# Kernel tuning notes

Hardware: AMD Instinct MI355X
Metric: run time of the kernel (lower is better)

Reference implementation:

```python
import jax, jax.numpy as jnp
import numpy as np

N = 6000          # nodes
E = 192000        # edges (avg degree 32)
D = 512           # input_dim
H = 512           # hidden_dim
O = 40            # output_dim (classes)
K = 4096          # codebook_size
LAMB_EDGE = 1.0
LAMB_NODE = 1.0
COMMIT_W = 0.25
EPS = 1e-12


def _graph_conv(x, W, b, src, dst):
    """DGL GraphConv with norm='both' + ReLU activation.
    out = relu( D_in^{-1/2} A D_out^{-1/2} x W + b )"""
    ones = jnp.ones((E,), x.dtype)
    deg_out = jnp.clip(jax.ops.segment_sum(ones, src, num_segments=N), 1.0)
    deg_in = jnp.clip(jax.ops.segment_sum(ones, dst, num_segments=N), 1.0)
    xs = x * jax.lax.rsqrt(deg_out)[:, None]          # scale by src out-degree
    agg = jax.ops.segment_sum(xs[src], dst, num_segments=N)  # gather-scatter
    agg = agg * jax.lax.rsqrt(deg_in)[:, None]        # scale by dst in-degree
    return jax.nn.relu(agg @ W + b)


def _l2norm(x):
    return x * jax.lax.rsqrt(jnp.sum(x * x, axis=-1, keepdims=True) + EPS)


def setup_inputs() -> dict:
    key = jax.random.key(0)
    ks = jax.random.split(key, 13)
    s = lambda d: 1.0 / np.sqrt(d)
    return {
        "feats": jax.random.normal(ks[0], (N, D), jnp.float32),
        "W1": jax.random.normal(ks[1], (D, D), jnp.float32) * s(D),
        "b1": jnp.zeros((D,), jnp.float32),
        "W2": jax.random.normal(ks[2], (D, H), jnp.float32) * s(D),
        "b2": jnp.zeros((H,), jnp.float32),
        "Wd1": jax.random.normal(ks[3], (D, D), jnp.float32) * s(D),
        "bd1": jnp.zeros((D,), jnp.float32),
        "Wd2": jax.random.normal(ks[4], (D, D), jnp.float32) * s(D),
        "bd2": jnp.zeros((D,), jnp.float32),
        "Wl": jax.random.normal(ks[5], (H, O), jnp.float32) * s(H),
        "bl": jnp.zeros((O,), jnp.float32),
        "codebook": jax.random.normal(ks[6], (K, D), jnp.float32),
        "src": jax.random.randint(ks[7], (E,), 0, N, jnp.int32),
        "dst": jax.random.randint(ks[8], (E,), 0, N, jnp.int32),
    }


def reference(feats, W1, b1, W2, b2, Wd1, bd1, Wd2, bd2, Wl, bl, codebook, src, dst):
    # dense adjacency (as the torch module materializes via to_dense())
    adj = jnp.zeros((N, N), feats.dtype).at[dst, src].add(1.0)

    # GraphConv layer 1 (dropout is identity in eval)
    h = _graph_conv(feats, W1, b1, src, dst)           # [N, D]

    # cosine-sim VectorQuantize
    hn = _l2norm(h)
    en = _l2norm(codebook)                             # [K, D]
    dist = hn @ en.T                                   # [N, K] cosine sims
    ind = jnp.argmax(dist, axis=-1)                    # [N]
    q = en[ind]                                        # quantize with normed codebook
    commit_loss = COMMIT_W * jnp.mean((jax.lax.stop_gradient(q) - h) ** 2)
    quantized = h + jax.lax.stop_gradient(q - h)       # straight-through

    quantized_edge = quantized @ Wd1 + bd1             # decoder_1
    quantized_node = quantized @ Wd2 + bd2             # decoder_2

    feature_rec_loss = LAMB_NODE * jnp.mean((h - quantized_node) ** 2)

    adj_q = quantized_edge @ quantized_edge.T          # [N, N]
    adj_q = (adj_q - adj_q.min()) / (adj_q.max() - adj_q.min())
    edge_rec_loss = LAMB_EDGE * jnp.sqrt(jnp.mean((adj - adj_q) ** 2))

    # GraphConv layer 2 + output linear
    h2 = _graph_conv(quantized_edge, W2, b2, src, dst) # [N, H]
    out = h2 @ Wl + bl                                 # [N, O]

    loss = feature_rec_loss + edge_rec_loss + commit_loss
    return out, loss, dist
```

## Files before the change

### kernel.cpp

```cpp
#include <hip/hip_runtime.h>

typedef unsigned int u32;
typedef unsigned long long u64;

#define NN_ 6000
#define EE_ 192000
#define DD_ 512
#define KK_ 4096
#define OO_ 40
#define HSZ (1 << 19)
#define HMASK (HSZ - 1)
#define MT_A 376
#define NB_N 47

typedef __bf16 bf16x8 __attribute__((ext_vector_type(8)));
typedef float f32x4 __attribute__((ext_vector_type(4)));

__device__ __forceinline__ u32 okey(float f) {
    u32 u = __float_as_uint(f);
    return (u & 0x80000000u) ? ~u : (u | 0x80000000u);
}
__device__ __forceinline__ float dkey(u32 u) {
    u32 b = (u & 0x80000000u) ? (u ^ 0x80000000u) : ~u;
    return __uint_as_float(b);
}
__device__ __forceinline__ u64 packKey(float v, int col) {
    return ((u64)okey(v) << 32) | (u32)(~(u32)col);
}
__device__ __forceinline__ unsigned short f2bf_rne(float f) {
    u32 x = __float_as_uint(f);
    u32 r = x + 0x7fffu + ((x >> 16) & 1u);
    return (unsigned short)(r >> 16);
}
__device__ __forceinline__ void gld_lds16(void* l, const void* g) {
    __builtin_amdgcn_global_load_lds(
        (const __attribute__((address_space(1))) unsigned int*)g,
        (__attribute__((address_space(3))) unsigned int*)l, 16, 0, 0);
}
#define LGKM0 do { asm volatile("s_waitcnt lgkmcnt(0)" ::: "memory"); __builtin_amdgcn_sched_barrier(0); } while (0)

__global__ void k_deg(const int* __restrict__ src, const int* __restrict__ dst,
                      int* __restrict__ degout, int* __restrict__ degin) {
    int e = blockIdx.x * 256 + threadIdx.x;
    if (e >= EE_) return;
    atomicAdd(&degout[src[e]], 1);
    atomicAdd(&degin[dst[e]], 1);
}

__global__ void k_rsqrtdeg(const int* __restrict__ degout, const int* __restrict__ degin,
                           float* __restrict__ rout, float* __restrict__ rin) {
    int i = blockIdx.x * 256 + threadIdx.x;
    if (i >= NN_) return;
    int doV = degout[i]; if (doV < 1) doV = 1;
    int diV = degin[i];  if (diV < 1) diV = 1;
    rout[i] = rsqrtf((float)doV);
    rin[i]  = rsqrtf((float)diV);
}

__global__ void k_scan(const int* __restrict__ cnt, int* __restrict__ offs, int n) {
    __shared__ int buf[1024];
    __shared__ int carry;
    if (threadIdx.x == 0) { carry = 0; offs[0] = 0; }
    __syncthreads();
    for (int base = 0; base < n; base += 1024) {
        int i = base + threadIdx.x;
        int v = (i < n) ? cnt[i] : 0;
        buf[threadIdx.x] = v;
        __syncthreads();
        for (int off = 1; off < 1024; off <<= 1) {
            int t = (threadIdx.x >= off) ? buf[threadIdx.x - off] : 0;
            __syncthreads();
            buf[threadIdx.x] += t;
            __syncthreads();
        }
        if (i < n) offs[i + 1] = carry + buf[threadIdx.x];
        __syncthreads();
        if (threadIdx.x == 0) carry += buf[1023];
        __syncthreads();
    }
}

__global__ void k_fill(const int* __restrict__ src, const int* __restrict__ dst,
                       const int* __restrict__ offs, int* __restrict__ cursor,
                       int* __restrict__ esrc) {
    int e = blockIdx.x * 256 + threadIdx.x;
    if (e >= EE_) return;
    int d = dst[e];
    int pos = offs[d] + atomicAdd(&cursor[d], 1);
    esrc[pos] = src[e];
}

__device__ __forceinline__ void split8(const float* vals, uint4& hw, uint4& lw) {
    u32 h[4], l[4];
    #pragma unroll
    for (int j = 0; j < 4; ++j) {
        unsigned short h0 = f2bf_rne(vals[2*j]),   h1 = f2bf_rne(vals[2*j+1]);
        float hf0 = __uint_as_float((u32)h0 << 16), hf1 = __uint_as_float((u32)h1 << 16);
        unsigned short l0 = f2bf_rne(vals[2*j] - hf0), l1 = f2bf_rne(vals[2*j+1] - hf1);
        h[j] = (u32)h0 | ((u32)h1 << 16);
        l[j] = (u32)l0 | ((u32)l1 << 16);
    }
    hw = make_uint4(h[0], h[1], h[2], h[3]);
    lw = make_uint4(l[0], l[1], l[2], l[3]);
}

template<int UNW>
__global__ __launch_bounds__(256) void k_aggs(
    const float* __restrict__ X, const int* __restrict__ esrc,
    const int* __restrict__ offs, const float* __restrict__ rout,
    const float* __restrict__ rin,
    unsigned short* __restrict__ dh, unsigned short* __restrict__ dl,
    float* __restrict__ gacc) {
    __shared__ float packbuf[4][128];
    __shared__ float mred[4];
    int b = blockIdx.x;
    int xcd = b & 7;
    int slice = xcd >> 1;
    int w = threadIdx.x >> 6, lane = threadIdx.x & 63;
    int wid = ((((b >> 3) << 1) | (xcd & 1)) << 2) + w;
    const float* Xc = X + slice * 128 + lane * 2;
    float mrAcc = 0.f;
    for (int node = wid; node < NN_; node += 1024) {
        int beg = offs[node], end = offs[node + 1];
        float a0 = 0.f, a1 = 0.f, u0 = 0.f, u1 = 0.f;
        for (int e = beg; e < end; ) {
            int cnt = end - e; if (cnt > 64) cnt = 64;
            int sreg = 0; float wreg = 0.f;
            if (lane < cnt) { sreg = esrc[e + lane]; wreg = rout[sreg]; }
            int j = 0;
            for (; j + 4 <= cnt; j += 4) {
                int s0 = __shfl(sreg, j),     s1 = __shfl(sreg, j + 1);
                int s2 = __shfl(sreg, j + 2), s3 = __shfl(sreg, j + 3);
                float w0 = __shfl(wreg, j),     w1 = __shfl(wreg, j + 1);
                float w2 = __shfl(wreg, j + 2), w3 = __shfl(wreg, j + 3);
                float2 v0 = *(const float2*)(Xc + (size_t)s0 * DD_);
                float2 v1 = *(const float2*)(Xc + (size_t)s1 * DD_);
                float2 v2 = *(const float2*)(Xc + (size_t)s2 * DD_);
                float2 v3 = *(const float2*)(Xc + (size_t)s3 * DD_);
                a0 = fmaf(w0, v0.x, a0); a1 = fmaf(w0, v0.y, a1);
                a0 = fmaf(w1, v1.x, a0); a1 = fmaf(w1, v1.y, a1);
                a0 = fmaf(w2, v2.x, a0); a1 = fmaf(w2, v2.y, a1);
                a0 = fmaf(w3, v3.x, a0); a1 = fmaf(w3, v3.y, a1);
                if (UNW) {
                    u0 += (v0.x + v1.x) + (v2.x + v3.x);
                    u1 += (v0.y + v1.y) + (v2.y + v3.y);
                }
            }
            for (; j < cnt; ++j) {
                int sj = __shfl(sreg, j); float wj = __shfl(wreg, j);
                float2 v = *(const float2*)(Xc + (size_t)sj * DD_);
                a0 = fmaf(wj, v.x, a0); a1 = fmaf(wj, v.y, a1);
                if (UNW) { u0 += v.x; u1 += v.y; }
            }
            e += cnt;
        }
        float ri = rin[node];
        packbuf[w][lane * 2] = a0 * ri;
        packbuf[w][lane * 2 + 1] = a1 * ri;
        LGKM0;
        if (lane < 16) {
            uint4 hw, lw;
            split8(&packbuf[w][(lane >> 2) * 32 + (lane & 3) * 8], hw, lw);
            int kb = slice * 4 + (lane >> 2);
            int lo = (lane & 3) * 16 + (node & 15);
            size_t base = (((size_t)(node >> 4) * 16 + kb) * 64 + lo) * 8;
            *(uint4*)(dh + base) = hw;
            *(uint4*)(dl + base) = lw;
        }
        if (UNW) {
            float2 q = *(const float2*)(Xc + (size_t)node * DD_);
            mrAcc = fmaf(q.x, u0, mrAcc);
            mrAcc = fmaf(q.y, u1, mrAcc);
        }
    }
    if (UNW) {
        for (int off = 32; off; off >>= 1) mrAcc += __shfl_xor(mrAcc, off);
        if (lane == 0) mred[w] = mrAcc;
        __syncthreads();
        if (threadIdx.x == 0)
            atomicAdd(&gacc[5], mred[0] + mred[1] + mred[2] + mred[3]);
    }
}

__global__ __launch_bounds__(256) void k_cbscale(const float* __restrict__ cb,
                                                 float* __restrict__ scale, int nrows) {
    int w = threadIdx.x >> 6, lane = threadIdx.x & 63;
    for (int row = blockIdx.x * 4 + w; row < nrows; row += gridDim.x * 4) {
        const float4* p = (const float4*)(cb + (size_t)row * DD_);
        float4 x = p[lane], y = p[lane + 64];
        float s = x.x * x.x + x.y * x.y + x.z * x.z + x.w * x.w
                + y.x * y.x + y.y * y.y + y.z * y.z + y.w * y.w;
        for (int off = 32; off; off >>= 1) s += __shfl_xor(s, off);
        if (lane == 0) scale[row] = 1.0f / sqrtf(s + 1e-12f);
    }
}

__global__ __launch_bounds__(256) void k_pack(
    const float* __restrict__ src, const float* __restrict__ rowscale,
    const int* __restrict__ gidx, int nrows,
    unsigned short* __restrict__ dh, unsigned short* __restrict__ dl) {
    int u = threadIdx.x >> 6, lane = threadIdx.x & 63;
    int nmt = (nrows + 15) >> 4;
    for (int unit = blockIdx.x; unit < nmt * 4; unit += gridDim.x) {
        int mt = unit >> 2, kb = (unit & 3) * 4 + u;
        int gr = mt * 16 + (lane & 15);
        int k = kb * 32 + (lane >> 4) * 8;
        float vals[8] = {0.f,0.f,0.f,0.f,0.f,0.f,0.f,0.f};
        if (gr < nrows) {
            int row = gidx ? gidx[gr] : gr;
            float sc = rowscale ? rowscale[row] : 1.0f;
            const float4* p = (const float4*)(src + (size_t)row * DD_ + k);
            float4 a = p[0], bv = p[1];
            vals[0]=a.x*sc; vals[1]=a.y*sc; vals[2]=a.z*sc; vals[3]=a.w*sc;
            vals[4]=bv.x*sc; vals[5]=bv.y*sc; vals[6]=bv.z*sc; vals[7]=bv.w*sc;
        }
        uint4 hw, lw;
        split8(vals, hw, lw);
        size_t base = (((size_t)mt * 16 + kb) * 64 + lane) * 8;
        *(uint4*)(dh + base) = hw;
        *(uint4*)(dl + base) = lw;
    }
}

__global__ __launch_bounds__(256) void k_wpack(
    const float* __restrict__ W,
    unsigned short* __restrict__ dh, unsigned short* __restrict__ dl) {
    int u = threadIdx.x >> 6, lane = threadIdx.x & 63;
    int mt = blockIdx.x, kb = blockIdx.y * 4 + u;
    int n = mt * 16 + (lane & 15);
    int k = kb * 32 + (lane >> 4) * 8;
    float vals[8];
    #pragma unroll
    for (int j = 0; j < 8; ++j) vals[j] = W[(size_t)(k + j) * DD_ + n];
    uint4 hw, lw;
    split8(vals, hw, lw);
    size_t base = (((size_t)mt * 16 + kb) * 64 + lane) * 8;
    *(uint4*)(dh + base) = hw;
    *(uint4*)(dl + base) = lw;
}

template<int MODE>
__global__ __launch_bounds__(256) void gemm_mfma(
    const unsigned short* __restrict__ Ah, const unsigned short* __restrict__ Al,
    const unsigned short* __restrict__ Bh, const unsigned short* __restrict__ Bl,
    float* __restrict__ Cout, const float* __restrict__ bias,
    const float* __restrict__ Ref, int relu, int Mrows,
    float* __restrict__ gacc, u32* __restrict__ minKey, u32* __restrict__ maxKey) {
    if (MODE == 1 && blockIdx.x < blockIdx.y) return;
    __shared__ char lds[32768];
    int tid = threadIdx.x;
    int wave = tid >> 6, lane = tid & 63;
    int gmtA = blockIdx.y * 8, gmtB = blockIdx.x * 8;
    const unsigned short* garr; int gmt0;
    if (wave == 0)      { garr = Ah; gmt0 = gmtA; }
    else if (wave == 1) { garr = Al; gmt0 = gmtA; }
    else if (wave == 2) { garr = Bh; gmt0 = gmtB; }
    else                { garr = Bl; gmt0 = gmtB; }
    char* ldst = lds + wave * 8192;
    f32x4 acc[4][4];
    #pragma unroll
    for (int i = 0; i < 4; ++i)
        #pragma unroll
        for (int j = 0; j < 4; ++j) acc[i][j] = (f32x4){0.f, 0.f, 0.f, 0.f};
    int wm = wave >> 1, wn = wave & 1;
    for (int kb = 0; kb < 16; ++kb) {
        #pragma unroll
        for (int t = 0; t < 8; ++t) {
            const char* g = (const char*)garr + (((size_t)(gmt0 + t) * 16 + kb) * 1024) + lane * 16;
            gld_lds16(ldst + t * 1024 + lane * 16, g);
        }
        __syncthreads();
        bf16x8 a_h[4], a_l[4], b_h[4], b_l[4];
        #pragma unroll
        for (int i = 0; i < 4; ++i) {
            int at = wm * 4 + i, bt = wn * 4 + i;
            a_h[i] = *(const bf16x8*)(lds + 0     + at * 1024 + lane * 16);
            a_l[i] = *(const bf16x8*)(lds + 8192  + at * 1024 + lane * 16);
            b_h[i] = *(const bf16x8*)(lds + 16384 + bt * 1024 + lane * 16);
            b_l[i] = *(const bf16x8*)(lds + 24576 + bt * 1024 + lane * 16);
        }
        #pragma unroll
        for (int i = 0; i < 4; ++i)
            #pragma unroll
            for (int j = 0; j < 4; ++j) {
                acc[i][j] = __builtin_amdgcn_mfma_f32_16x16x32_bf16(a_h[i], b_h[j], acc[i][j], 0, 0, 0);
                acc[i][j] = __builtin_amdgcn_mfma_f32_16x16x32_bf16(a_h[i], b_l[j], acc[i][j], 0, 0, 0);
                acc[i][j] = __builtin_amdgcn_mfma_f32_16x16x32_bf16(a_l[i], b_h[j], acc[i][j], 0, 0, 0);
            }
        __syncthreads();
    }
    int m_base = blockIdx.y * 128 + wm * 64;
    int n_base = blockIdx.x * 128 + wn * 64;
    int rq = lane >> 4, cc = lane & 15;
    if (MODE == 0) {
        #pragma unroll
        for (int i = 0; i < 4; ++i) {
            int m = m_base + i * 16 + rq * 4;
            #pragma unroll
            for (int j = 0; j < 4; ++j) {
                int n = n_base + j * 16 + cc;
                #pragma unroll
                for (int r = 0; r < 4; ++r) {
                    if (m + r < NN_) Cout[(size_t)(m + r) * KK_ + n] = acc[i][j][r];
                }
            }
        }
    } else if (MODE == 2) {
        #pragma unroll
        for (int i = 0; i < 4; ++i) {
            int m = m_base + i * 16 + rq * 4;
            #pragma unroll
            for (int j = 0; j < 4; ++j) {
                int n = n_base + j * 16 + cc;
                float bv = bias[n];
                #pragma unroll
                for (int r = 0; r < 4; ++r) {
                    if (m + r < Mrows) {
                        float v = acc[i][j][r] + bv;
                        if (relu) v = fmaxf(v, 0.f);
                        Cout[(size_t)(m + r) * DD_ + n] = v;
                    }
                }
            }
        }
    } else if (MODE == 3) {
        float s = 0.f;
        #pragma unroll
        for (int i = 0; i < 4; ++i) {
            int m = m_base + i * 16 + rq * 4;
            #pragma unroll
            for (int j = 0; j < 4; ++j) {
                int n = n_base + j * 16 + cc;
                float bv = bias[n];
                #pragma unroll
                for (int r = 0; r < 4; ++r) {
                    if (m + r < Mrows) {
                        float d = Ref[(size_t)(m + r) * DD_ + n] - (acc[i][j][r] + bv);
                        s = fmaf(d, d, s);
                    }
                }
            }
        }
        float* red = (float*)lds;
        red[tid] = s; __syncthreads();
        for (int st = 128; st; st >>= 1) { if (tid < st) red[tid] += red[tid + st]; __syncthreads(); }
        if (tid == 0) atomicAdd(&gacc[3], red[0]);
    } else {
        float tsum = 0.f, tsq = 0.f, tmin = 3.4e38f, tmax = -3.4e38f;
        #pragma unroll
        for (int i = 0; i < 4; ++i) {
            #pragma unroll
            for (int j = 0; j < 4; ++j) {
                #pragma unroll
                for (int r = 0; r < 4; ++r) {
                    int m = m_base + i * 16 + rq * 4 + r;
                    int n = n_base + j * 16 + cc;
                    if (m < NN_ && n < NN_ && n >= m) {
                        float v = acc[i][j][r];
                        float w = (n > m) ? 2.f : 1.f;
                        tsum += w * v;
                        tsq  += w * v * v;
                        tmin = fminf(tmin, v);
                        tmax = fmaxf(tmax, v);
                    }
                }
            }
        }
        float* red = (float*)lds;
        red[tid] = tsum; __syncthreads();
        for (int s = 128; s; s >>= 1) { if (tid < s) red[tid] += red[tid + s]; __syncthreads(); }
        if (tid == 0) atomicAdd(&gacc[0], red[0]);
        __syncthreads();
        red[tid] = tsq; __syncthreads();
        for (int s = 128; s; s >>= 1) { if (tid < s) red[tid] += red[tid + s]; __syncthreads(); }
        if (tid == 0) atomicAdd(&gacc[1], red[0]);
        __syncthreads();
        red[tid] = tmin; __syncthreads();
        for (int s = 128; s; s >>= 1) { if (tid < s) red[tid] = fminf(red[tid], red[tid + s]); __syncthreads(); }
        if (tid == 0) atomicMin(minKey, okey(red[0]));
        __syncthreads();
        red[tid] = tmax; __syncthreads();
        for (int s = 128; s; s >>= 1) { if (tid < s) red[tid] = fmaxf(red[tid], red[tid + s]); __syncthreads(); }
        if (tid == 0) atomicMax(maxKey, okey(red[0]));
    }
}

__global__ __launch_bounds__(256) void k_rescore(
    const float* __restrict__ dist, const float* __restrict__ h,
    const float* __restrict__ rnorm, const float* __restrict__ cb,
    const float* __restrict__ scale, int* __restrict__ ind) {
    int row = blockIdx.x;
    const float4* dr4 = (const float4*)(dist + (size_t)row * KK_);
    int tid = threadIdx.x;
    float4 vbuf[4];
    float lmax = -3.4e38f;
    #pragma unroll
    for (int it = 0; it < 4; ++it) {
        float4 v = dr4[tid + it * 256];
        vbuf[it] = v;
        lmax = fmaxf(fmaxf(fmaxf(v.x, v.y), fmaxf(v.z, v.w)), lmax);
    }
    for (int off = 32; off; off >>= 1) lmax = fmaxf(lmax, __shfl_xor(lmax, off));
    __shared__ float wm4[4];
    __shared__ float bmax;
    __shared__ int cnt;
    __shared__ int cand[32];
    __shared__ u64 best;
    int lane = tid & 63, wv = tid >> 6;
    if (lane == 0) wm4[wv] = lmax;
    if (tid == 0) { cnt = 0; best = 0; }
    __syncthreads();
    if (tid == 0) bmax = fmaxf(fmaxf(wm4[0], wm4[1]), fmaxf(wm4[2], wm4[3]));
    __syncthreads();
    float thr = bmax - 1e-3f;
    #pragma unroll
    for (int it = 0; it < 4; ++it) {
        float4 v = vbuf[it];
        int cbase = (tid + it * 256) * 4;
        if (v.x >= thr) { int p = atomicAdd(&cnt, 1); if (p < 32) cand[p] = cbase + 0; }
        if (v.y >= thr) { int p = atomicAdd(&cnt, 1); if (p < 32) cand[p] = cbase + 1; }
        if (v.z >= thr) { int p = atomicAdd(&cnt, 1); if (p < 32) cand[p] = cbase + 2; }
        if (v.w >= thr) { int p = atomicAdd(&cnt, 1); if (p < 32) cand[p] = cbase + 3; }
    }
    __syncthreads();
    int nc = min(cnt, 32);
    float hr = rnorm[row];
    const float* hp = h + (size_t)row * DD_;
    for (int c = wv; c < nc; c += 4) {
        int col = cand[c];
        const float* cp = cb + (size_t)col * DD_;
        float dot = 0.f;
        #pragma unroll
        for (int j = 0; j < 8; ++j) dot = fmaf(hp[lane + j * 64], cp[lane + j * 64], dot);
        for (int off = 32; off; off >>= 1) dot += __shfl_xor(dot, off);
        if (lane == 0) atomicMax(&best, packKey(dot * hr * scale[col], col));
    }
    __syncthreads();
    if (tid == 0) ind[row] = (int)(~(u32)(best & 0xFFFFFFFFull));
}

__global__ __launch_bounds__(256) void gemm_nn(
    const float* __restrict__ A, const float* __restrict__ B,
    const float* __restrict__ bias, float* __restrict__ C,
    int M, int Ncols, int Kdim) {
    __shared__ float As[16][68];
    __shared__ float Bs[16][68];
    int tid = threadIdx.x;
    int tx = tid & 15, ty = tid >> 4;
    int m0 = blockIdx.y * 64, n0 = blockIdx.x * 64;
    float cv[4][4] = {};
    int ar = tid >> 2;
    int ak = (tid & 3) << 2;
    int am = m0 + ar;
    const float* Arow = (am < M) ? (A + (size_t)am * Kdim) : nullptr;
    int bk = tid >> 4;
    int bn = (tid & 15) << 2;
    for (int k0 = 0; k0 < Kdim; k0 += 16) {
        float4 av = make_float4(0.f, 0.f, 0.f, 0.f);
        if (Arow) av = *(const float4*)(Arow + k0 + ak);
        As[ak + 0][ar] = av.x; As[ak + 1][ar] = av.y;
        As[ak + 2][ar] = av.z; As[ak + 3][ar] = av.w;
        float4 bv = make_float4(0.f, 0.f, 0.f, 0.f);
        if (n0 + bn < Ncols)
            bv = *(const float4*)(B + (size_t)(k0 + bk) * Ncols + n0 + bn);
        Bs[bk][bn + 0] = bv.x; Bs[bk][bn + 1] = bv.y;
        Bs[bk][bn + 2] = bv.z; Bs[bk][bn + 3] = bv.w;
        __syncthreads();
        #pragma unroll
        for (int kk = 0; kk < 16; ++kk) {
            float4 a4 = *(const float4*)&As[kk][ty << 2];
            float4 b4 = *(const float4*)&Bs[kk][tx << 2];
            float ax[4] = {a4.x, a4.y, a4.z, a4.w};
            float bx[4] = {b4.x, b4.y, b4.z, b4.w};
            #pragma unroll
            for (int i = 0; i < 4; ++i)
                #pragma unroll
                for (int j = 0; j < 4; ++j)
                    cv[i][j] = fmaf(ax[i], bx[j], cv[i][j]);
        }
        __syncthreads();
    }
    #pragma unroll
    for (int i = 0; i < 4; ++i) {
        int m = m0 + (ty << 2) + i;
        if (m >= M) continue;
        #pragma unroll
        for (int j = 0; j < 4; ++j) {
            int n = n0 + (tx << 2) + j;
            if (n >= Ncols) continue;
            C[(size_t)m * Ncols + n] = cv[i][j] + bias[n];
        }
    }
}

__global__ __launch_bounds__(256) void k_losses(
    const float* __restrict__ h, const float* __restrict__ cb,
    const float* __restrict__ scale, const int* __restrict__ ind,
    float* __restrict__ gacc) {
    float s1 = 0.f;
    for (int idx = blockIdx.x * 256 + threadIdx.x; idx < NN_ * DD_; idx += gridDim.x * 256) {
        int m = idx >> 9, d = idx & 511;
        int r = ind[m];
        float q = cb[(size_t)r * DD_ + d] * scale[r];
        float dq = q - h[idx];
        s1 = fmaf(dq, dq, s1);
    }
    for (int off = 32; off; off >>= 1) s1 += __shfl_xor(s1, off);
    __shared__ float w1[4];
    int lane = threadIdx.x & 63, wv = threadIdx.x >> 6;
    if (lane == 0) w1[wv] = s1;
    __syncthreads();
    if (threadIdx.x == 0) atomicAdd(&gacc[2], w1[0] + w1[1] + w1[2] + w1[3]);
}

__global__ void k_hash(const int* __restrict__ src, const int* __restrict__ dst,
                       int* __restrict__ hkey, int* __restrict__ hcnt) {
    int e = blockIdx.x * 256 + threadIdx.x;
    if (e >= EE_) return;
    int key = dst[e] * NN_ + src[e];
    u32 h = ((u32)key * 2654435761u) & HMASK;
    while (true) {
        int old = atomicCAS(&hkey[h], -1, key);
        if (old == -1 || old == key) { atomicAdd(&hcnt[h], 1); break; }
        h = (h + 1) & HMASK;
    }
}

__global__ __launch_bounds__(256) void k_m2scan(const int* __restrict__ hcnt, float* __restrict__ gacc) {
    float s = 0.f;
    for (int i = blockIdx.x * 256 + threadIdx.x; i < HSZ; i += gridDim.x * 256) {
        float c = (float)hcnt[i];
        s = fmaf(c, c, s);
    }
    for (int off = 32; off; off >>= 1) s += __shfl_xor(s, off);
    __shared__ float w1[4];
    int lane = threadIdx.x & 63, wv = threadIdx.x >> 6;
    if (lane == 0) w1[wv] = s;
    __syncthreads();
    if (threadIdx.x == 0) atomicAdd(&gacc[4], w1[0] + w1[1] + w1[2] + w1[3]);
}

__global__ void k_final(const float* __restrict__ gacc, const u32* __restrict__ minKey,
                        const u32* __restrict__ maxKey, float* __restrict__ lossOut) {
    if (threadIdx.x != 0 || blockIdx.x != 0) return;
    double Rsum = gacc[0], Rsq = gacc[1], commitS = gacc[2], recS = gacc[3];
    double m2 = gacc[4], mr = gacc[5], ms = (double)EE_;
    double mn = (double)dkey(*minKey);
    double mx = (double)dkey(*maxKey);
    double den = mx - mn;
    double NN2 = (double)NN_ * (double)NN_;
    double sum_aq2 = (Rsq - 2.0 * mn * Rsum + NN2 * mn * mn) / (den * den);
    double sum_maq = (mr - mn * ms) / den;
    double total = sum_aq2 + m2 - 2.0 * sum_maq;
    double edge = sqrt(total / NN2);
    double commit = 0.25 * commitS / ((double)NN_ * (double)DD_);
    double rec = recS / ((double)NN_ * (double)DD_);
    *lossOut = (float)(rec + edge + commit);
}

extern "C" void kernel_launch(void* const* d_in, const int* in_sizes, int n_in,
                              void* d_out, int out_size, void* d_ws, size_t ws_size,
                              hipStream_t stream) {
    const float* feats = (const float*)d_in[0];
    const float* W1 = (const float*)d_in[1];
    const float* b1 = (const float*)d_in[2];
    const float* W2 = (const float*)d_in[3];
    const float* b2v = (const float*)d_in[4];
    const float* Wd1 = (const float*)d_in[5];
    const float* bd1 = (const float*)d_in[6];
    const float* Wd2 = (const float*)d_in[7];
    const float* bd2 = (const float*)d_in[8];
    const float* Wl = (const float*)d_in[9];
    const float* bl = (const float*)d_in[10];
    const float* cb = (const float*)d_in[11];
    const int* src = (const int*)d_in[12];
    const int* dst = (const int*)d_in[13];

    float* outF = (float*)d_out;
    float* lossOut = outF + (size_t)NN_ * OO_;
    float* distOut = lossOut + 1;

    char* w = (char*)d_ws;
    size_t off = 0;
    auto alloc = [&](size_t bytes) -> void* {
        void* p = w + off;
        off = (off + bytes + 255) & ~(size_t)255;
        return p;
    };
    float* gacc = (float*)alloc(64);
    u32* maxKey = (u32*)alloc(4);
    int* degin = (int*)alloc((size_t)NN_ * 4);
    int* degout = (int*)alloc((size_t)NN_ * 4);
    int* cursor = (int*)alloc((size_t)NN_ * 4);
    int* hcnt = (int*)alloc((size_t)HSZ * 4);
    size_t z0end = off;
    int* hkey = (int*)alloc((size_t)HSZ * 4);
    u32* minKey = (u32*)alloc(4);
    size_t z1end = off;
    int* offs = (int*)alloc((size_t)(NN_ + 1) * 4);
    int* esrc = (int*)alloc((size_t)EE_ * 4);
    float* rin = (float*)alloc((size_t)NN_ * 4);
    float* rout = (float*)alloc((size_t)NN_ * 4);
    int* ind = (int*)alloc((size_t)NN_ * 4);
    float* scale = (float*)alloc((size_t)KK_ * 4);
    float* rnorm = (float*)alloc((size_t)NN_ * 4);
    float* h = (float*)alloc((size_t)NN_ * DD_ * 4);
    float* QE = (float*)alloc((size_t)NN_ * DD_ * 4);
    const size_t NPACK = (size_t)MT_A * 16 * DD_;
    unsigned short* P1 = (unsigned short*)alloc(NPACK * 2 * 2);
    unsigned short* P2 = (unsigned short*)alloc(NPACK * 2 * 2);
    unsigned short* enp = (unsigned short*)alloc((size_t)KK_ * DD_ * 2 * 2);
    const size_t WPACK = (size_t)32 * 16 * DD_;
    unsigned short* W1p = (unsigned short*)alloc(WPACK * 2 * 2);
    unsigned short* Wd1p = (unsigned short*)alloc(WPACK * 2 * 2);
    unsigned short* Wd2p = (unsigned short*)alloc(WPACK * 2 * 2);
    unsigned short* W2p = (unsigned short*)alloc(WPACK * 2 * 2);

    unsigned short* aggp_h = P1,  *aggp_l = P1 + NPACK;
    unsigned short* qcp_h  = P1,  *qcp_l  = P1 + NPACK;
    unsigned short* ag2p_h = P1,  *ag2p_l = P1 + NPACK;
    unsigned short* hnp_h  = P2,  *hnp_l  = P2 + NPACK;
    unsigned short* QEp_h  = P2,  *QEp_l  = P2 + NPACK;
    unsigned short* enp_h  = enp, *enp_l  = enp + (size_t)KK_ * DD_;

    hipMemsetAsync(w, 0, z0end, stream);
    hipMemsetAsync(w + z0end, 0xFF, z1end - z0end, stream);

    const int TB = 256;
    k_deg<<<(EE_ + TB - 1) / TB, TB, 0, stream>>>(src, dst, degout, degin);
    k_rsqrtdeg<<<(NN_ + TB - 1) / TB, TB, 0, stream>>>(degout, degin, rout, rin);
    k_scan<<<1, 1024, 0, stream>>>(degin, offs, NN_);
    k_fill<<<(EE_ + TB - 1) / TB, TB, 0, stream>>>(src, dst, offs, cursor, esrc);
    k_wpack<<<dim3(32, 4), TB, 0, stream>>>(W1, W1p, W1p + WPACK);
    k_wpack<<<dim3(32, 4), TB, 0, stream>>>(Wd1, Wd1p, Wd1p + WPACK);
    k_wpack<<<dim3(32, 4), TB, 0, stream>>>(Wd2, Wd2p, Wd2p + WPACK);
    k_wpack<<<dim3(32, 4), TB, 0, stream>>>(W2, W2p, W2p + WPACK);
    k_aggs<0><<<1024, TB, 0, stream>>>(feats, esrc, offs, rout, rin, aggp_h, aggp_l, nullptr);
    gemm_mfma<2><<<dim3(4, NB_N), TB, 0, stream>>>(aggp_h, aggp_l, W1p, W1p + WPACK,
                                                   h, b1, nullptr, 1, NN_, nullptr, nullptr, nullptr);
    k_cbscale<<<256, TB, 0, stream>>>(h, rnorm, NN_);
    k_cbscale<<<256, TB, 0, stream>>>(cb, scale, KK_);
    k_pack<<<512, TB, 0, stream>>>(h, rnorm, nullptr, NN_, hnp_h, hnp_l);
    k_pack<<<512, TB, 0, stream>>>(cb, scale, nullptr, KK_, enp_h, enp_l);
    gemm_mfma<0><<<dim3(KK_ / 128, NB_N), TB, 0, stream>>>(hnp_h, hnp_l, enp_h, enp_l,
                                                           distOut, nullptr, nullptr, 0, NN_,
                                                           nullptr, nullptr, nullptr);
    k_rescore<<<NN_, TB, 0, stream>>>(distOut, h, rnorm, cb, scale, ind);
    k_pack<<<512, TB, 0, stream>>>(cb, scale, ind, NN_, qcp_h, qcp_l);
    gemm_mfma<2><<<dim3(4, NB_N), TB, 0, stream>>>(qcp_h, qcp_l, Wd1p, Wd1p + WPACK,
                                                   QE, bd1, nullptr, 0, NN_, nullptr, nullptr, nullptr);
    gemm_mfma<3><<<dim3(4, NB_N), TB, 0, stream>>>(qcp_h, qcp_l, Wd2p, Wd2p + WPACK,
                                                   nullptr, bd2, h, 0, NN_, gacc, nullptr, nullptr);
    k_losses<<<2048, TB, 0, stream>>>(h, cb, scale, ind, gacc);
    k_pack<<<512, TB, 0, stream>>>(QE, nullptr, nullptr, NN_, QEp_h, QEp_l);
    gemm_mfma<1><<<dim3(NB_N, NB_N), TB, 0, stream>>>(QEp_h, QEp_l, QEp_h, QEp_l,
                                                      nullptr, nullptr, nullptr, 0, NN_,
                                                      gacc, minKey, maxKey);
    k_hash<<<(EE_ + TB - 1) / TB, TB, 0, stream>>>(src, dst, hkey, hcnt);
    k_m2scan<<<512, TB, 0, stream>>>(hcnt, gacc);
    k_aggs<1><<<1024, TB, 0, stream>>>(QE, esrc, offs, rout, rin, ag2p_h, ag2p_l, gacc);
    gemm_mfma<2><<<dim3(4, NB_N), TB, 0, stream>>>(ag2p_h, ag2p_l, W2p, W2p + WPACK,
                                                   h, b2v, nullptr, 1, NN_, nullptr, nullptr, nullptr);
    gemm_nn<<<dim3(1, 94), TB, 0, stream>>>(h, Wl, bl, outF, NN_, OO_, DD_);
    k_final<<<1, 64, 0, stream>>>(gacc, minKey, maxKey, lossOut);
}
```

Baseline: 688.5 us.

## Use two-term split GEMM for cosine dist, triangular grid, wave-per-row rescore

Adds a template flag so the distance GEMM computes only the hi*hi and hi*lo bf16 products and skips loading the A low part, cutting MFMA work and global loads by about a third. The symmetric adjacency GEMM now launches only the lower-triangular blocks via an index mapping instead of launching the full grid and exiting early. The rescore kernel is rewritten so each wave handles one row with ballot-based candidate enumeration, removing shared-memory atomics and block syncs. The reduced-precision distances may shift argmax ties and change the written dist values slightly, but candidates are rescored in fp32.

Result: slower. 710.8 us (+3.2%).

```diff
diff --git a/kernel.cpp b/kernel.cpp
--- a/kernel.cpp
+++ b/kernel.cpp
@@ -239,18 +239,25 @@
     *(uint4*)(dl + base) = lw;
 }
 
-template<int MODE>
+template<int MODE, int THREE>
 __global__ __launch_bounds__(256) void gemm_mfma(
     const unsigned short* __restrict__ Ah, const unsigned short* __restrict__ Al,
     const unsigned short* __restrict__ Bh, const unsigned short* __restrict__ Bl,
     float* __restrict__ Cout, const float* __restrict__ bias,
     const float* __restrict__ Ref, int relu, int Mrows,
     float* __restrict__ gacc, u32* __restrict__ minKey, u32* __restrict__ maxKey) {
-    if (MODE == 1 && blockIdx.x < blockIdx.y) return;
+    int bx, by;
+    if (MODE == 1) {
+        int t = blockIdx.x;
+        int bi = (int)((sqrtf(8.f * (float)t + 1.f) - 1.f) * 0.5f);
+        while ((bi + 1) * (bi + 2) / 2 <= t) ++bi;
+        while (bi * (bi + 1) / 2 > t) --bi;
+        bx = bi; by = t - bi * (bi + 1) / 2;
+    } else { bx = blockIdx.x; by = blockIdx.y; }
     __shared__ char lds[32768];
     int tid = threadIdx.x;
     int wave = tid >> 6, lane = tid & 63;
-    int gmtA = blockIdx.y * 8, gmtB = blockIdx.x * 8;
+    int gmtA = by * 8, gmtB = bx * 8;
     const unsigned short* garr; int gmt0;
     if (wave == 0)      { garr = Ah; gmt0 = gmtA; }
     else if (wave == 1) { garr = Al; gmt0 = gmtA; }
@@ -264,10 +271,12 @@
         for (int j = 0; j < 4; ++j) acc[i][j] = (f32x4){0.f, 0.f, 0.f, 0.f};
     int wm = wave >> 1, wn = wave & 1;
     for (int kb = 0; kb < 16; ++kb) {
-        #pragma unroll
-        for (int t = 0; t < 8; ++t) {
-            const char* g = (const char*)garr + (((size_t)(gmt0 + t) * 16 + kb) * 1024) + lane * 16;
-            gld_lds16(ldst + t * 1024 + lane * 16, g);
+        if (THREE || wave != 1) {
+            #pragma unroll
+            for (int t = 0; t < 8; ++t) {
+                const char* g = (const char*)garr + (((size_t)(gmt0 + t) * 16 + kb) * 1024) + lane * 16;
+                gld_lds16(ldst + t * 1024 + lane * 16, g);
+            }
         }
         __syncthreads();
         bf16x8 a_h[4], a_l[4], b_h[4], b_l[4];
@@ -275,7 +284,7 @@
         for (int i = 0; i < 4; ++i) {
             int at = wm * 4 + i, bt = wn * 4 + i;
             a_h[i] = *(const bf16x8*)(lds + 0     + at * 1024 + lane * 16);
-            a_l[i] = *(const bf16x8*)(lds + 8192  + at * 1024 + lane * 16);
+            if (THREE) a_l[i] = *(const bf16x8*)(lds + 8192 + at * 1024 + lane * 16);
             b_h[i] = *(const bf16x8*)(lds + 16384 + bt * 1024 + lane * 16);
             b_l[i] = *(const bf16x8*)(lds + 24576 + bt * 1024 + lane * 16);
         }
@@ -285,12 +294,13 @@
             for (int j = 0; j < 4; ++j) {
                 acc[i][j] = __builtin_amdgcn_mfma_f32_16x16x32_bf16(a_h[i], b_h[j], acc[i][j], 0, 0, 0);
                 acc[i][j] = __builtin_amdgcn_mfma_f32_16x16x32_bf16(a_h[i], b_l[j], acc[i][j], 0, 0, 0);
-                acc[i][j] = __builtin_amdgcn_mfma_f32_16x16x32_bf16(a_l[i], b_h[j], acc[i][j], 0, 0, 0);
-            }
-        __syncthreads();
-    }
-    int m_base = blockIdx.y * 128 + wm * 64;
-    int n_base = blockIdx.x * 128 + wn * 64;
+                if (THREE)
+                    acc[i][j] = __builtin_amdgcn_mfma_f32_16x16x32_bf16(a_l[i], b_h[j], acc[i][j], 0, 0, 0);
+            }
+        __syncthreads();
+    }
+    int m_base = by * 128 + wm * 64;
+    int n_base = bx * 128 + wn * 64;
     int rq = lane >> 4, cc = lane & 15;
     if (MODE == 0) {
         #pragma unroll
@@ -389,54 +399,49 @@
     const float* __restrict__ dist, const float* __restrict__ h,
     const float* __restrict__ rnorm, const float* __restrict__ cb,
     const float* __restrict__ scale, int* __restrict__ ind) {
-    int row = blockIdx.x;
-    const float4* dr4 = (const float4*)(dist + (size_t)row * KK_);
-    int tid = threadIdx.x;
-    float4 vbuf[4];
-    float lmax = -3.4e38f;
-    #pragma unroll
-    for (int it = 0; it < 4; ++it) {
-        float4 v = dr4[tid + it * 256];
-        vbuf[it] = v;
-        lmax = fmaxf(fmaxf(fmaxf(v.x, v.y), fmaxf(v.z, v.w)), lmax);
-    }
-    for (int off = 32; off; off >>= 1) lmax = fmaxf(lmax, __shfl_xor(lmax, off));
-    __shared__ float wm4[4];
-    __shared__ float bmax;
-    __shared__ int cnt;
-    __shared__ int cand[32];
-    __shared__ u64 best;
-    int lane = tid & 63, wv = tid >> 6;
-    if (lane == 0) wm4[wv] = lmax;
-    if (tid == 0) { cnt = 0; best = 0; }
-    __syncthreads();
-    if (tid == 0) bmax = fmaxf(fmaxf(wm4[0], wm4[1]), fmaxf(wm4[2], wm4[3]));
-    __syncthreads();
-    float thr = bmax - 1e-3f;
-    #pragma unroll
-    for (int it = 0; it < 4; ++it) {
-        float4 v = vbuf[it];
-        int cbase = (tid + it * 256) * 4;
-        if (v.x >= thr) { int p = atomicAdd(&cnt, 1); if (p < 32) cand[p] = cbase + 0; }
-        if (v.y >= thr) { int p = atomicAdd(&cnt, 1); if (p < 32) cand[p] = cbase + 1; }
-        if (v.z >= thr) { int p = atomicAdd(&cnt, 1); if (p < 32) cand[p] = cbase + 2; }
-        if (v.w >= thr) { int p = atomicAdd(&cnt, 1); if (p < 32) cand[p] = cbase + 3; }
-    }
-    __syncthreads();
-    int nc = min(cnt, 32);
-    float hr = rnorm[row];
-    const float* hp = h + (size_t)row * DD_;
-    for (int c = wv; c < nc; c += 4) {
-        int col = cand[c];
-        const float* cp = cb + (size_t)col * DD_;
-        float dot = 0.f;
-        #pragma unroll
-        for (int j = 0; j < 8; ++j) dot = fmaf(hp[lane + j * 64], cp[lane + j * 64], dot);
-        for (int off = 32; off; off >>= 1) dot += __shfl_xor(dot, off);
-        if (lane == 0) atomicMax(&best, packKey(dot * hr * scale[col], col));
-    }
-    __syncthreads();
-    if (tid == 0) ind[row] = (int)(~(u32)(best & 0xFFFFFFFFull));
+    int w = threadIdx.x >> 6, lane = threadIdx.x & 63;
+    for (int row = blockIdx.x * 4 + w; row < NN_; row += gridDim.x * 4) {
+        const float4* dr4 = (const float4*)(dist + (size_t)row * KK_);
+        float4 vbuf[16];
+        float lmax = -3.4e38f;
+        #pragma unroll
+        for (int it = 0; it < 16; ++it) {
+            float4 v = dr4[lane + it * 64];
+            vbuf[it] = v;
+            lmax = fmaxf(lmax, fmaxf(fmaxf(v.x, v.y), fmaxf(v.z, v.w)));
+        }
+        for (int off = 32; off; off >>= 1) lmax = fmaxf(lmax, __shfl_xor(lmax, off));
+        float thr = lmax - 1e-3f;
+        float hr = rnorm[row];
+        const float* hp = h + (size_t)row * DD_;
+        u64 best = 0;
+        #pragma unroll 1
+        for (int it = 0; it < 16; ++it) {
+            float4 v = vbuf[it];
+            u32 m4 = (v.x >= thr ? 1u : 0u) | (v.y >= thr ? 2u : 0u)
+                   | (v.z >= thr ? 4u : 0u) | (v.w >= thr ? 8u : 0u);
+            u64 bal = __ballot(m4 != 0);
+            while (bal) {
+                int l = __ffsll((unsigned long long)bal) - 1;
+                bal &= bal - 1;
+                u32 mm = __shfl(m4, l);
+                while (mm) {
+                    int j = __ffs(mm) - 1;
+                    mm &= mm - 1;
+                    int col = (l + it * 64) * 4 + j;
+                    const float* cp = cb + (size_t)col * DD_;
+                    float dot = 0.f;
+                    #pragma unroll
+                    for (int jj = 0; jj < 8; ++jj)
+                        dot = fmaf(hp[lane + jj * 64], cp[lane + jj * 64], dot);
+                    for (int off = 32; off; off >>= 1) dot += __shfl_xor(dot, off);
+                    u64 key = packKey(dot * hr * scale[col], col);
+                    if (key > best) best = key;
+                }
+            }
+        }
+        if (lane == 0) ind[row] = (int)(~(u32)(best & 0xFFFFFFFFull));
+    }
 }
 
 __global__ __launch_bounds__(256) void gemm_nn(
@@ -636,31 +641,31 @@
     k_wpack<<<dim3(32, 4), TB, 0, stream>>>(Wd2, Wd2p, Wd2p + WPACK);
     k_wpack<<<dim3(32, 4), TB, 0, stream>>>(W2, W2p, W2p + WPACK);
     k_aggs<0><<<1024, TB, 0, stream>>>(feats, esrc, offs, rout, rin, aggp_h, aggp_l, nullptr);
-    gemm_mfma<2><<<dim3(4, NB_N), TB, 0, stream>>>(aggp_h, aggp_l, W1p, W1p + WPACK,
-                                                   h, b1, nullptr, 1, NN_, nullptr, nullptr, nullptr);
+    gemm_mfma<2,1><<<dim3(4, NB_N), TB, 0, stream>>>(aggp_h, aggp_l, W1p, W1p + WPACK,
+                                                     h, b1, nullptr, 1, NN_, nullptr, nullptr, nullptr);
     k_cbscale<<<256, TB, 0, stream>>>(h, rnorm, NN_);
     k_cbscale<<<256, TB, 0, stream>>>(cb, scale, KK_);
     k_pack<<<512, TB, 0, stream>>>(h, rnorm, nullptr, NN_, hnp_h, hnp_l);
     k_pack<<<512, TB, 0, stream>>>(cb, scale, nullptr, KK_, enp_h, enp_l);
-    gemm_mfma<0><<<dim3(KK_ / 128, NB_N), TB, 0, stream>>>(hnp_h, hnp_l, enp_h, enp_l,
-                                                           distOut, nullptr, nullptr, 0, NN_,
-                                                           nullptr, nullptr, nullptr);
-    k_rescore<<<NN_, TB, 0, stream>>>(distOut, h, rnorm, cb, scale, ind);
+    gemm_mfma<0,0><<<dim3(KK_ / 128, NB_N), TB, 0, stream>>>(hnp_h, hnp_l, enp_h, enp_l,
+                                                             distOut, nullptr, nullptr, 0, NN_,
+                                                             nullptr, nullptr, nullptr);
+    k_rescore<<<1024, TB, 0, stream>>>(distOut, h, rnorm, cb, scale, ind);
     k_pack<<<512, TB, 0, stream>>>(cb, scale, ind, NN_, qcp_h, qcp_l);
-    gemm_mfma<2><<<dim3(4, NB_N), TB, 0, stream>>>(qcp_h, qcp_l, Wd1p, Wd1p + WPACK,
-                                                   QE, bd1, nullptr, 0, NN_, nullptr, nullptr, nullptr);
-    gemm_mfma<3><<<dim3(4, NB_N), TB, 0, stream>>>(qcp_h, qcp_l, Wd2p, Wd2p + WPACK,
-                                                   nullptr, bd2, h, 0, NN_, gacc, nullptr, nullptr);
+    gemm_mfma<2,1><<<dim3(4, NB_N), TB, 0, stream>>>(qcp_h, qcp_l, Wd1p, Wd1p + WPACK,
+                                                     QE, bd1, nullptr, 0, NN_, nullptr, nullptr, nullptr);
+    gemm_mfma<3,1><<<dim3(4, NB_N), TB, 0, stream>>>(qcp_h, qcp_l, Wd2p, Wd2p + WPACK,
+                                                     nullptr, bd2, h, 0, NN_, gacc, nullptr, nullptr);
     k_losses<<<2048, TB, 0, stream>>>(h, cb, scale, ind, gacc);
     k_pack<<<512, TB, 0, stream>>>(QE, nullptr, nullptr, NN_, QEp_h, QEp_l);
-    gemm_mfma<1><<<dim3(NB_N, NB_N), TB, 0, stream>>>(QEp_h, QEp_l, QEp_h, QEp_l,
-                                                      nullptr, nullptr, nullptr, 0, NN_,
-                                                      gacc, minKey, maxKey);
+    gemm_mfma<1,1><<<NB_N * (NB_N + 1) / 2, TB, 0, stream>>>(QEp_h, QEp_l, QEp_h, QEp_l,
+                                                             nullptr, nullptr, nullptr, 0, NN_,
+                                                             gacc, minKey, maxKey);
     k_hash<<<(EE_ + TB - 1) / TB, TB, 0, stream>>>(src, dst, hkey, hcnt);
     k_m2scan<<<512, TB, 0, stream>>>(hcnt, gacc);
     k_aggs<1><<<1024, TB, 0, stream>>>(QE, esrc, offs, rout, rin, ag2p_h, ag2p_l, gacc);
-    gemm_mfma<2><<<dim3(4, NB_N), TB, 0, stream>>>(ag2p_h, ag2p_l, W2p, W2p + WPACK,
-                                                   h, b2v, nullptr, 1, NN_, nullptr, nullptr, nullptr);
+    gemm_mfma<2,1><<<dim3(4, NB_N), TB, 0, stream>>>(ag2p_h, ag2p_l, W2p, W2p + WPACK,
+                                                     h, b2v, nullptr, 1, NN_, nullptr, nullptr, nullptr);
     gemm_nn<<<dim3(1, 94), TB, 0, stream>>>(h, Wl, bl, outF, NN_, OO_, DD_);
     k_final<<<1, 64, 0, stream>>>(gacc, minKey, maxKey, lossOut);
 }
```
